# Kernel tuning notes

Hardware: AMD Instinct MI355X
Metric: run time of the kernel (lower is better)

Reference implementation:

```python
import jax, jax.numpy as jnp
import numpy as np

D = 1024
N_HEADS = 16
D_HEAD = D // N_HEADS


def setup_inputs() -> dict:
    key = jax.random.key(0)
    ks = jax.random.split(key, 7)
    B, S = 4, 1024
    x = jax.random.normal(ks[0], (B, S, D), dtype=jnp.float32)
    # per-head linear params, stacked over heads: W[h] is [d_head, d_head] (torch Linear weight),
    # y = s @ W[h].T + b[h]
    scale = 1.0 / np.sqrt(D_HEAD)
    Wq = jax.random.uniform(ks[1], (N_HEADS, D_HEAD, D_HEAD), jnp.float32, -scale, scale)
    Wk = jax.random.uniform(ks[2], (N_HEADS, D_HEAD, D_HEAD), jnp.float32, -scale, scale)
    Wv = jax.random.uniform(ks[3], (N_HEADS, D_HEAD, D_HEAD), jnp.float32, -scale, scale)
    bq = jax.random.uniform(ks[4], (N_HEADS, D_HEAD), jnp.float32, -scale, scale)
    bk = jax.random.uniform(ks[5], (N_HEADS, D_HEAD), jnp.float32, -scale, scale)
    bv = jax.random.uniform(ks[6], (N_HEADS, D_HEAD), jnp.float32, -scale, scale)
    return {"pix_sequences": x, "Wq": Wq, "Wk": Wk, "Wv": Wv,
            "bq": bq, "bk": bk, "bv": bv}


def reference(pix_sequences, Wq, Wk, Wv, bq, bk, bv):
    B, S, d = pix_sequences.shape
    # split feature dim into heads: [B, S, H, dh]
    xh = pix_sequences.reshape(B, S, N_HEADS, D_HEAD)
    # per-head linear: y = s @ W.T + b
    q = jnp.einsum('bshd,hed->bshe', xh, Wq) + bq  # [B,S,H,dh]
    k = jnp.einsum('bshd,hed->bshe', xh, Wk) + bk
    v = jnp.einsum('bshd,hed->bshe', xh, Wv) + bv
    scores = jnp.einsum('bqhd,bkhd->bhqk', q, k) / jnp.sqrt(jnp.float32(D_HEAD))
    attn = jax.nn.softmax(scores, axis=-1)  # [B,H,S,S]
    out = jnp.einsum('bhqk,bkhd->bqhd', attn, v)  # [B,S,H,dh]
    return out.reshape(B, S, d)
```

## Files before the change

### kernel.cpp

```cpp
#include <hip/hip_runtime.h>
#include <hip/hip_bf16.h>

constexpr int BB = 4;
constexpr int SS = 1024;
constexpr int HH = 16;
constexpr int DH = 64;
constexpr int DM = 1024;

using f32x16 = __attribute__((ext_vector_type(16))) float;
using s16x8  = __attribute__((ext_vector_type(8))) short;

__device__ __forceinline__ f32x16 mfma32(s16x8 a, s16x8 b, f32x16 c) {
    return __builtin_amdgcn_mfma_f32_32x32x16_bf16(a, b, c, 0, 0, 0);
}

__device__ __forceinline__ unsigned short bf16bits(float x) {
    union { __hip_bfloat16 h; unsigned short s; } cv;
    cv.h = __float2bfloat16(x);
    return cv.s;
}
__device__ __forceinline__ unsigned pk_bf16(float lo, float hi) {
    return (unsigned)bf16bits(lo) | ((unsigned)bf16bits(hi) << 16);
}

__device__ __forceinline__ float fast_exp2(float x) {
#if __has_builtin(__builtin_amdgcn_exp2f)
    return __builtin_amdgcn_exp2f(x);
#else
    return __expf(x * 0.6931471805599453f);
#endif
}

__device__ __forceinline__ int kperm(int g) {
    const int m = g & 12;
    return (m == 4 || m == 8) ? (g ^ 12) : g;
}

__global__ __launch_bounds__(256) void qkv_proj_kernel(
    const float* __restrict__ x,
    const float* __restrict__ Wq, const float* __restrict__ Wk, const float* __restrict__ Wv,
    const float* __restrict__ bq, const float* __restrict__ bk, const float* __restrict__ bv,
    __hip_bfloat16* __restrict__ q_ws, __hip_bfloat16* __restrict__ k_ws,
    __hip_bfloat16* __restrict__ v_ws)
{
    const int bid  = blockIdx.x;
    const int tile = bid & 7;
    const int pair = bid >> 3;
    const int b = pair >> 4, h = pair & 15;
    const int t = threadIdx.x;
    const int w = t >> 6, l = t & 63;
    const int lq = l & 31, hi = l >> 5;
    const int s0 = tile * 128;

    __shared__ __align__(16) char Xs[16384];
    __shared__ __align__(16) char Kt[16384];
    __shared__ __align__(16) char Vt[16384];

    {
        const float* xb = x + (size_t)(b * SS + s0) * DM + h * DH;
        #pragma unroll
        for (int i = 0; i < 8; ++i) {
            const int c  = t + 256 * i;
            const int r  = c >> 4, cw = c & 15;
            float4 v4 = *reinterpret_cast<const float4*>(xb + (size_t)r * DM + cw * 4);
            uint2 p;
            p.x = pk_bf16(v4.x, v4.y);
            p.y = pk_bf16(v4.z, v4.w);
            *reinterpret_cast<uint2*>(Xs + r * 128 + ((cw * 8) ^ ((r & 7) << 4))) = p;
        }
    }
    __syncthreads();

    const int arow = w * 32 + lq;
    const int asw  = (arow & 7) << 4;
    s16x8 af[4];
    #pragma unroll
    for (int s = 0; s < 4; ++s)
        af[s] = *reinterpret_cast<const s16x8*>(Xs + arow * 128 + ((s * 32 + hi * 16) ^ asw));
    __syncthreads();

    #pragma unroll
    for (int m = 0; m < 3; ++m) {
        const float* Wm = (m == 0) ? Wq : (m == 1) ? Wk : Wv;
        const float* bm = (m == 0) ? bq : (m == 1) ? bk : bv;

        f32x16 a0, a1;
        #pragma unroll
        for (int r = 0; r < 16; ++r) { a0[r] = 0.0f; a1[r] = 0.0f; }

        #pragma unroll
        for (int s = 0; s < 4; ++s) {
            const float* wp0 = Wm + (size_t)(h * DH + lq) * DH + s * 16 + hi * 8;
            const float* wp1 = wp0 + 32 * DH;
            float4 wa0 = reinterpret_cast<const float4*>(wp0)[0];
            float4 wb0 = reinterpret_cast<const float4*>(wp0)[1];
            float4 wa1 = reinterpret_cast<const float4*>(wp1)[0];
            float4 wb1 = reinterpret_cast<const float4*>(wp1)[1];
            union { unsigned u[4]; s16x8 v; } bf0, bf1;
            bf0.u[0] = pk_bf16(wa0.x, wa0.y); bf0.u[1] = pk_bf16(wa0.z, wa0.w);
            bf0.u[2] = pk_bf16(wb0.x, wb0.y); bf0.u[3] = pk_bf16(wb0.z, wb0.w);
            bf1.u[0] = pk_bf16(wa1.x, wa1.y); bf1.u[1] = pk_bf16(wa1.z, wa1.w);
            bf1.u[2] = pk_bf16(wb1.x, wb1.y); bf1.u[3] = pk_bf16(wb1.z, wb1.w);
            a0 = mfma32(af[s], bf0.v, a0);
            a1 = mfma32(af[s], bf1.v, a1);
        }

        const float bias0 = bm[h * DH + lq];
        const float bias1 = bm[h * DH + 32 + lq];

        if (m < 2) {
            char* T = (m == 0) ? Xs : Kt;
            #pragma unroll
            for (int r = 0; r < 16; ++r) {
                const int row = w * 32 + (r & 3) + 8 * (r >> 2) + 4 * hi;
                const int sw  = (row & 7) << 4;
                *reinterpret_cast<unsigned short*>(T + row * 128 + ((lq * 2) ^ sw)) =
                    bf16bits(a0[r] + bias0);
                *reinterpret_cast<unsigned short*>(T + row * 128 + (((32 + lq) * 2) ^ sw)) =
                    bf16bits(a1[r] + bias1);
            }
        } else {
            #pragma unroll
            for (int g = 0; g < 4; ++g) {
                const int off = w * 64 + g * 16 + hi * 8;
                uint2 p0, p1;
                p0.x = pk_bf16(a0[4*g+0] + bias0, a0[4*g+1] + bias0);
                p0.y = pk_bf16(a0[4*g+2] + bias0, a0[4*g+3] + bias0);
                p1.x = pk_bf16(a1[4*g+0] + bias1, a1[4*g+1] + bias1);
                p1.y = pk_bf16(a1[4*g+2] + bias1, a1[4*g+3] + bias1);
                *reinterpret_cast<uint2*>(Vt + lq * 256 + (off ^ ((lq & 7) << 4))) = p0;
                *reinterpret_cast<uint2*>(Vt + (32 + lq) * 256 + (off ^ (((32 + lq) & 7) << 4))) = p1;
            }
        }
    }
    __syncthreads();

    #pragma unroll
    for (int i = 0; i < 4; ++i) {
        const int c   = t + 256 * i;
        const int row = c >> 3, cc = c & 7;
        const int off = row * 128 + ((cc * 16) ^ ((row & 7) << 4));
        s16x8 qv = *reinterpret_cast<const s16x8*>(Xs + off);
        *reinterpret_cast<s16x8*>(q_ws + ((size_t)pair * SS + s0 + row) * DH + cc * 8) = qv;
        s16x8 kv = *reinterpret_cast<const s16x8*>(Kt + off);
        *reinterpret_cast<s16x8*>(k_ws + ((size_t)pair * SS + s0 + row) * DH + cc * 8) = kv;
    }
    #pragma unroll
    for (int i = 0; i < 4; ++i) {
        const int c   = t + 256 * i;
        const int row = c >> 4, cc = c & 15;
        s16x8 vv = *reinterpret_cast<const s16x8*>(
            Vt + row * 256 + ((cc * 16) ^ ((row & 7) << 4)));
        *reinterpret_cast<s16x8*>(v_ws + ((size_t)pair * DH + row) * SS + s0 + cc * 8) = vv;
    }
}

__global__ __launch_bounds__(512, 4) void attn_kernel(
    const __hip_bfloat16* __restrict__ q_ws,
    const __hip_bfloat16* __restrict__ k_ws,
    const __hip_bfloat16* __restrict__ v_ws,
    float* __restrict__ out)
{
    const int bid  = blockIdx.x;
    const int lbid = (bid & 7) * 64 + (bid >> 3);
    const int qt   = lbid & 7;
    const int pair = lbid >> 3;
    const int b = pair >> 4, h = pair & 15;
    const int t = threadIdx.x;
    const int w = t >> 6, l = t & 63;
    const int lq = l & 31, hi = l >> 5;
    const int qg = w & 3, p = w >> 2;

    __shared__ __align__(16) char smem[33792];

    const __hip_bfloat16* qp =
        q_ws + ((size_t)pair * SS + qt * 128 + qg * 32 + lq) * DH + hi * 8;
    s16x8 qf[4];
    #pragma unroll
    for (int s5 = 0; s5 < 4; ++s5)
        qf[s5] = *reinterpret_cast<const s16x8*>(qp + s5 * 16);

    const int u0 = t, u1 = t + 512;
    const __hip_bfloat16* kb = k_ws + (size_t)pair * SS * DH;
    const __hip_bfloat16* vb = v_ws + (size_t)pair * DH * SS;

    const int r0g = (u0 >> 3) & 31, r0m = r0g & 12;
    const int pr0 = (u0 >> 3 & ~31) | ((r0m == 4 || r0m == 8) ? (r0g ^ 12) : r0g);
    const int kOff0 = pr0 * 128 + (((u0 & 7) ^ (pr0 & 7)) << 4);
    const int r1g = (u1 >> 3) & 31, r1m = r1g & 12;
    const int pr1 = (u1 >> 3 & ~31) | ((r1m == 4 || r1m == 8) ? (r1g ^ 12) : r1g);
    const int kOff1 = pr1 * 128 + (((u1 & 7) ^ (pr1 & 7)) << 4);

    const int vOff0 = (u0 >> 4) * 256 + (((u0 & 15) ^ ((u0 >> 4) & 15)) << 4);
    const int vOff1 = (u1 >> 4) * 256 + (((u1 & 15) ^ ((u1 >> 4) & 15)) << 4);
    const size_t vs0 = (size_t)(u0 >> 4) * SS + (u0 & 15) * 8;
    const size_t vs1 = (size_t)(u1 >> 4) * SS + (u1 & 15) * 8;

    {
        s16x8 k0 = *reinterpret_cast<const s16x8*>(kb + u0 * 8);
        s16x8 k1 = *reinterpret_cast<const s16x8*>(kb + u1 * 8);
        s16x8 v0 = *reinterpret_cast<const s16x8*>(vb + vs0);
        s16x8 v1 = *reinterpret_cast<const s16x8*>(vb + vs1);
        *reinterpret_cast<s16x8*>(smem + kOff0) = k0;
        *reinterpret_cast<s16x8*>(smem + kOff1) = k1;
        *reinterpret_cast<s16x8*>(smem + 16384 + vOff0) = v0;
        *reinterpret_cast<s16x8*>(smem + 16384 + vOff1) = v1;
    }
    __syncthreads();

    f32x16 o0, o1, lacc;
    #pragma unroll
    for (int r = 0; r < 16; ++r) { o0[r] = 0.0f; o1[r] = 0.0f; lacc[r] = 0.0f; }
    const float cml = 0.18033688011112042f;

    const int kbase0 = (p * 64 + lq) * 128;
    const int kbase1 = kbase0 + 32 * 128;
    const int swzK = (lq & 7) << 4;
    const int swzV = (lq & 15) << 4;
    const int vrow0 = lq * 256, vrow1 = (32 + lq) * 256;

    s16x8 kr0, kr1, vr0, vr1;
    for (int st = 0; st < 8; ++st) {
        if (st < 7) {
            kr0 = *reinterpret_cast<const s16x8*>(kb + (st + 1) * 8192 + u0 * 8);
            kr1 = *reinterpret_cast<const s16x8*>(kb + (st + 1) * 8192 + u1 * 8);
            vr0 = *reinterpret_cast<const s16x8*>(vb + vs0 + (st + 1) * 128);
            vr1 = *reinterpret_cast<const s16x8*>(vb + vs1 + (st + 1) * 128);
        }
        const char* Kp = smem;
        const char* Vp = smem + 16384;

        f32x16 sc0, sc1;
        #pragma unroll
        for (int r = 0; r < 16; ++r) { sc0[r] = 0.0f; sc1[r] = 0.0f; }
        #pragma unroll
        for (int s5 = 0; s5 < 4; ++s5) {
            const int co = (2 * s5 + hi) << 4;
            s16x8 ka = *reinterpret_cast<const s16x8*>(Kp + kbase0 + (co ^ swzK));
            sc0 = mfma32(ka, qf[s5], sc0);
        }
        #pragma unroll
        for (int s5 = 0; s5 < 4; ++s5) {
            const int co = (2 * s5 + hi) << 4;
            s16x8 ka = *reinterpret_cast<const s16x8*>(Kp + kbase1 + (co ^ swzK));
            sc1 = mfma32(ka, qf[s5], sc1);
        }

        #pragma unroll
        for (int r = 0; r < 16; ++r) {
            sc0[r] = fast_exp2(sc0[r] * cml);
            sc1[r] = fast_exp2(sc1[r] * cml);
            lacc[r] += sc0[r] + sc1[r];
        }

        #pragma unroll
        for (int s5 = 0; s5 < 4; ++s5) {
            const int base = (s5 & 1) * 8;
            union { unsigned u[4]; s16x8 v; } afr;
            if (s5 < 2) {
                afr.u[0] = pk_bf16(sc0[base + 0], sc0[base + 1]);
                afr.u[1] = pk_bf16(sc0[base + 2], sc0[base + 3]);
                afr.u[2] = pk_bf16(sc0[base + 4], sc0[base + 5]);
                afr.u[3] = pk_bf16(sc0[base + 6], sc0[base + 7]);
            } else {
                afr.u[0] = pk_bf16(sc1[base + 0], sc1[base + 1]);
                afr.u[1] = pk_bf16(sc1[base + 2], sc1[base + 3]);
                afr.u[2] = pk_bf16(sc1[base + 4], sc1[base + 5]);
                afr.u[3] = pk_bf16(sc1[base + 6], sc1[base + 7]);
            }
            const int co = (2 * s5 + hi) << 4;
            s16x8 vb0 = *reinterpret_cast<const s16x8*>(Vp + vrow0 + ((p * 128 + co) ^ swzV));
            o0 = mfma32(afr.v, vb0, o0);
            s16x8 vb1 = *reinterpret_cast<const s16x8*>(Vp + vrow1 + ((p * 128 + co) ^ swzV));
            o1 = mfma32(afr.v, vb1, o1);
        }

        __syncthreads();
        if (st < 7) {
            *reinterpret_cast<s16x8*>(smem + kOff0) = kr0;
            *reinterpret_cast<s16x8*>(smem + kOff1) = kr1;
            *reinterpret_cast<s16x8*>(smem + 16384 + vOff0) = vr0;
            *reinterpret_cast<s16x8*>(smem + 16384 + vOff1) = vr1;
            __syncthreads();
        }
    }

    float ts[16];
    #pragma unroll
    for (int r = 0; r < 16; ++r) ts[r] = lacc[r];
    #pragma unroll
    for (int s = 8; s >= 1; s >>= 1)
        #pragma unroll
        for (int r = 0; r < 8; ++r)
            if (r < s) ts[r] += ts[r + s];
    const float lsum = ts[0] + __shfl_xor(ts[0], 32);

    float* Obuf = reinterpret_cast<float*>(smem + qg * 8192);
    float* mlb  = reinterpret_cast<float*>(smem + 32768 + qg * 256);
    if (p == 1) {
        #pragma unroll
        for (int r = 0; r < 16; ++r) {
            const int qr = (r & 3) + 8 * (r >> 2) + 4 * hi;
            Obuf[qr * 64 + lq]      = o0[r];
            Obuf[qr * 64 + 32 + lq] = o1[r];
        }
        mlb[lq] = lsum;
    }
    __syncthreads();
    if (p == 0) {
        const float inv = 1.0f / (lsum + mlb[lq]);
        #pragma unroll
        for (int r = 0; r < 16; ++r) {
            const int qr = (r & 3) + 8 * (r >> 2) + 4 * hi;
            const float invr = __shfl(inv, qr);
            float* op = out + ((size_t)b * SS + qt * 128 + qg * 32 + qr) * DM + h * DH + lq;
            op[0]  = (o0[r] + Obuf[qr * 64 + lq])      * invr;
            op[32] = (o1[r] + Obuf[qr * 64 + 32 + lq]) * invr;
        }
    }
}

extern "C" void kernel_launch(void* const* d_in, const int* in_sizes, int n_in,
                              void* d_out, int out_size, void* d_ws, size_t ws_size,
                              hipStream_t stream) {
    const float* x  = (const float*)d_in[0];
    const float* Wq = (const float*)d_in[1];
    const float* Wk = (const float*)d_in[2];
    const float* Wv = (const float*)d_in[3];
    const float* bq = (const float*)d_in[4];
    const float* bk = (const float*)d_in[5];
    const float* bv = (const float*)d_in[6];
    float* out = (float*)d_out;

    __hip_bfloat16* q_ws = (__hip_bfloat16*)d_ws;
    __hip_bfloat16* k_ws = q_ws + (size_t)BB * HH * SS * DH;
    __hip_bfloat16* v_ws = k_ws + (size_t)BB * HH * SS * DH;

    qkv_proj_kernel<<<dim3(BB * HH * (SS / 128)), dim3(256), 0, stream>>>(
        x, Wq, Wk, Wv, bq, bk, bv, q_ws, k_ws, v_ws);
    attn_kernel<<<dim3(BB * HH * (SS / 64 / 2)), dim3(512), 0, stream>>>(
        q_ws, k_ws, v_ws, out);
}
```

Measured before the change: 50.97 us.

## Halve projection tile to 64 rows, split output columns across waves, add MFMA priority hints

The QKV projection kernel now processes 64 sequence rows per block instead of 128, with the four waves arranged as 2 row groups by 2 output-column halves, each computing one 32x32 MFMA accumulator. This doubles the grid to 1024 blocks and shrinks shared memory and registers per block, aiming at better occupancy and load balance on the projection stage. Weight fragments are reloaded by more blocks in exchange. The attention kernel also wraps its two MFMA phases in s_setprio raises so waves in matrix work get issue priority over waves doing exp and stores.

```diff
diff --git a/kernel.cpp b/kernel.cpp
--- a/kernel.cpp
+++ b/kernel.cpp
@@ -44,22 +44,23 @@
     __hip_bfloat16* __restrict__ v_ws)
 {
     const int bid  = blockIdx.x;
-    const int tile = bid & 7;
-    const int pair = bid >> 3;
+    const int tile = bid & 15;
+    const int pair = bid >> 4;
     const int b = pair >> 4, h = pair & 15;
     const int t = threadIdx.x;
     const int w = t >> 6, l = t & 63;
     const int lq = l & 31, hi = l >> 5;
-    const int s0 = tile * 128;
-
-    __shared__ __align__(16) char Xs[16384];
-    __shared__ __align__(16) char Kt[16384];
-    __shared__ __align__(16) char Vt[16384];
+    const int rg = w & 1, eh = w >> 1;
+    const int s0 = tile * 64;
+
+    __shared__ __align__(16) char Xs[8192];
+    __shared__ __align__(16) char Kt[8192];
+    __shared__ __align__(16) char Vt[8192];
 
     {
         const float* xb = x + (size_t)(b * SS + s0) * DM + h * DH;
         #pragma unroll
-        for (int i = 0; i < 8; ++i) {
+        for (int i = 0; i < 4; ++i) {
             const int c  = t + 256 * i;
             const int r  = c >> 4, cw = c & 15;
             float4 v4 = *reinterpret_cast<const float4*>(xb + (size_t)r * DM + cw * 4);
@@ -71,72 +72,61 @@
     }
     __syncthreads();
 
-    const int arow = w * 32 + lq;
+    const int arow = rg * 32 + lq;
     const int asw  = (arow & 7) << 4;
     s16x8 af[4];
     #pragma unroll
     for (int s = 0; s < 4; ++s)
         af[s] = *reinterpret_cast<const s16x8*>(Xs + arow * 128 + ((s * 32 + hi * 16) ^ asw));
     __syncthreads();
+
+    const int e = eh * 32 + lq;
 
     #pragma unroll
     for (int m = 0; m < 3; ++m) {
         const float* Wm = (m == 0) ? Wq : (m == 1) ? Wk : Wv;
         const float* bm = (m == 0) ? bq : (m == 1) ? bk : bv;
 
-        f32x16 a0, a1;
-        #pragma unroll
-        for (int r = 0; r < 16; ++r) { a0[r] = 0.0f; a1[r] = 0.0f; }
+        f32x16 acc;
+        #pragma unroll
+        for (int r = 0; r < 16; ++r) acc[r] = 0.0f;
 
         #pragma unroll
         for (int s = 0; s < 4; ++s) {
-            const float* wp0 = Wm + (size_t)(h * DH + lq) * DH + s * 16 + hi * 8;
-            const float* wp1 = wp0 + 32 * DH;
-            float4 wa0 = reinterpret_cast<const float4*>(wp0)[0];
-            float4 wb0 = reinterpret_cast<const float4*>(wp0)[1];
-            float4 wa1 = reinterpret_cast<const float4*>(wp1)[0];
-            float4 wb1 = reinterpret_cast<const float4*>(wp1)[1];
-            union { unsigned u[4]; s16x8 v; } bf0, bf1;
-            bf0.u[0] = pk_bf16(wa0.x, wa0.y); bf0.u[1] = pk_bf16(wa0.z, wa0.w);
-            bf0.u[2] = pk_bf16(wb0.x, wb0.y); bf0.u[3] = pk_bf16(wb0.z, wb0.w);
-            bf1.u[0] = pk_bf16(wa1.x, wa1.y); bf1.u[1] = pk_bf16(wa1.z, wa1.w);
-            bf1.u[2] = pk_bf16(wb1.x, wb1.y); bf1.u[3] = pk_bf16(wb1.z, wb1.w);
-            a0 = mfma32(af[s], bf0.v, a0);
-            a1 = mfma32(af[s], bf1.v, a1);
-        }
-
-        const float bias0 = bm[h * DH + lq];
-        const float bias1 = bm[h * DH + 32 + lq];
+            const float* wp = Wm + (size_t)(h * DH + e) * DH + s * 16 + hi * 8;
+            float4 wa = reinterpret_cast<const float4*>(wp)[0];
+            float4 wb = reinterpret_cast<const float4*>(wp)[1];
+            union { unsigned u[4]; s16x8 v; } bf;
+            bf.u[0] = pk_bf16(wa.x, wa.y); bf.u[1] = pk_bf16(wa.z, wa.w);
+            bf.u[2] = pk_bf16(wb.x, wb.y); bf.u[3] = pk_bf16(wb.z, wb.w);
+            acc = mfma32(af[s], bf.v, acc);
+        }
+
+        const float bias = bm[h * DH + e];
 
         if (m < 2) {
             char* T = (m == 0) ? Xs : Kt;
             #pragma unroll
             for (int r = 0; r < 16; ++r) {
-                const int row = w * 32 + (r & 3) + 8 * (r >> 2) + 4 * hi;
-                const int sw  = (row & 7) << 4;
-                *reinterpret_cast<unsigned short*>(T + row * 128 + ((lq * 2) ^ sw)) =
-                    bf16bits(a0[r] + bias0);
-                *reinterpret_cast<unsigned short*>(T + row * 128 + (((32 + lq) * 2) ^ sw)) =
-                    bf16bits(a1[r] + bias1);
+                const int row = rg * 32 + (r & 3) + 8 * (r >> 2) + 4 * hi;
+                *reinterpret_cast<unsigned short*>(
+                    T + row * 128 + ((e * 2) ^ ((row & 7) << 4))) = bf16bits(acc[r] + bias);
             }
         } else {
             #pragma unroll
             for (int g = 0; g < 4; ++g) {
-                const int off = w * 64 + g * 16 + hi * 8;
-                uint2 p0, p1;
-                p0.x = pk_bf16(a0[4*g+0] + bias0, a0[4*g+1] + bias0);
-                p0.y = pk_bf16(a0[4*g+2] + bias0, a0[4*g+3] + bias0);
-                p1.x = pk_bf16(a1[4*g+0] + bias1, a1[4*g+1] + bias1);
-                p1.y = pk_bf16(a1[4*g+2] + bias1, a1[4*g+3] + bias1);
-                *reinterpret_cast<uint2*>(Vt + lq * 256 + (off ^ ((lq & 7) << 4))) = p0;
-                *reinterpret_cast<uint2*>(Vt + (32 + lq) * 256 + (off ^ (((32 + lq) & 7) << 4))) = p1;
+                const int off = rg * 64 + g * 16 + hi * 8;
+                uint2 p0;
+                p0.x = pk_bf16(acc[4*g+0] + bias, acc[4*g+1] + bias);
+                p0.y = pk_bf16(acc[4*g+2] + bias, acc[4*g+3] + bias);
+                *reinterpret_cast<uint2*>(Vt + e * 128 + (off ^ ((e & 7) << 4))) = p0;
             }
         }
     }
     __syncthreads();
 
     #pragma unroll
-    for (int i = 0; i < 4; ++i) {
+    for (int i = 0; i < 2; ++i) {
         const int c   = t + 256 * i;
         const int row = c >> 3, cc = c & 7;
         const int off = row * 128 + ((cc * 16) ^ ((row & 7) << 4));
@@ -144,13 +134,7 @@
         *reinterpret_cast<s16x8*>(q_ws + ((size_t)pair * SS + s0 + row) * DH + cc * 8) = qv;
         s16x8 kv = *reinterpret_cast<const s16x8*>(Kt + off);
         *reinterpret_cast<s16x8*>(k_ws + ((size_t)pair * SS + s0 + row) * DH + cc * 8) = kv;
-    }
-    #pragma unroll
-    for (int i = 0; i < 4; ++i) {
-        const int c   = t + 256 * i;
-        const int row = c >> 4, cc = c & 15;
-        s16x8 vv = *reinterpret_cast<const s16x8*>(
-            Vt + row * 256 + ((cc * 16) ^ ((row & 7) << 4)));
+        s16x8 vv = *reinterpret_cast<const s16x8*>(Vt + off);
         *reinterpret_cast<s16x8*>(v_ws + ((size_t)pair * DH + row) * SS + s0 + cc * 8) = vv;
     }
 }
@@ -233,6 +217,7 @@
         f32x16 sc0, sc1;
         #pragma unroll
         for (int r = 0; r < 16; ++r) { sc0[r] = 0.0f; sc1[r] = 0.0f; }
+        __builtin_amdgcn_s_setprio(1);
         #pragma unroll
         for (int s5 = 0; s5 < 4; ++s5) {
             const int co = (2 * s5 + hi) << 4;
@@ -245,6 +230,7 @@
             s16x8 ka = *reinterpret_cast<const s16x8*>(Kp + kbase1 + (co ^ swzK));
             sc1 = mfma32(ka, qf[s5], sc1);
         }
+        __builtin_amdgcn_s_setprio(0);
 
         #pragma unroll
         for (int r = 0; r < 16; ++r) {
@@ -253,6 +239,7 @@
             lacc[r] += sc0[r] + sc1[r];
         }
 
+        __builtin_amdgcn_s_setprio(1);
         #pragma unroll
         for (int s5 = 0; s5 < 4; ++s5) {
             const int base = (s5 & 1) * 8;
@@ -274,6 +261,7 @@
             s16x8 vb1 = *reinterpret_cast<const s16x8*>(Vp + vrow1 + ((p * 128 + co) ^ swzV));
             o1 = mfma32(afr.v, vb1, o1);
         }
+        __builtin_amdgcn_s_setprio(0);
 
         __syncthreads();
         if (st < 7) {
@@ -336,7 +324,7 @@
     __hip_bfloat16* k_ws = q_ws + (size_t)BB * HH * SS * DH;
     __hip_bfloat16* v_ws = k_ws + (size_t)BB * HH * SS * DH;
 
-    qkv_proj_kernel<<<dim3(BB * HH * (SS / 128)), dim3(256), 0, stream>>>(
+    qkv_proj_kernel<<<dim3(BB * HH * (SS / 64)), dim3(256), 0, stream>>>(
         x, Wq, Wk, Wv, bq, bk, bv, q_ws, k_ws, v_ws);
     attn_kernel<<<dim3(BB * HH * (SS / 64 / 2)), dim3(512), 0, stream>>>(
         q_ws, k_ws, v_ws, out);
```

After: 54.28 us. 1.07x slower.

## Double-buffer K/V tiles in shared memory to remove per-step barrier

Applied to the files above, without the earlier changes.

Grows LDS to two 32KB K/V buffers and alternates between them each step. The next tile's prefetched registers are written to the other buffer mid-iteration, after the softmax exponentials, which removes the second __syncthreads per step and the serialized store phase. In exchange LDS per block roughly doubles to about 65KB. With 512-thread blocks and launch_bounds(512,4), this may cut how many blocks fit on a CU and so lower occupancy.

```diff
diff --git a/kernel.cpp b/kernel.cpp
--- a/kernel.cpp
+++ b/kernel.cpp
@@ -171,7 +171,7 @@
     const int lq = l & 31, hi = l >> 5;
     const int qg = w & 3, p = w >> 2;
 
-    __shared__ __align__(16) char smem[33792];
+    __shared__ __align__(16) char smem[66560];
 
     const __hip_bfloat16* qp =
         q_ws + ((size_t)pair * SS + qt * 128 + qg * 32 + lq) * DH + hi * 8;
@@ -191,8 +191,8 @@
     const int pr1 = (u1 >> 3 & ~31) | ((r1m == 4 || r1m == 8) ? (r1g ^ 12) : r1g);
     const int kOff1 = pr1 * 128 + (((u1 & 7) ^ (pr1 & 7)) << 4);
 
-    const int vOff0 = (u0 >> 4) * 256 + (((u0 & 15) ^ ((u0 >> 4) & 15)) << 4);
-    const int vOff1 = (u1 >> 4) * 256 + (((u1 & 15) ^ ((u1 >> 4) & 15)) << 4);
+    const int vOff0 = 16384 + (u0 >> 4) * 256 + (((u0 & 15) ^ ((u0 >> 4) & 15)) << 4);
+    const int vOff1 = 16384 + (u1 >> 4) * 256 + (((u1 & 15) ^ ((u1 >> 4) & 15)) << 4);
     const size_t vs0 = (size_t)(u0 >> 4) * SS + (u0 & 15) * 8;
     const size_t vs1 = (size_t)(u1 >> 4) * SS + (u1 & 15) * 8;
 
@@ -203,8 +203,8 @@
         s16x8 v1 = *reinterpret_cast<const s16x8*>(vb + vs1);
         *reinterpret_cast<s16x8*>(smem + kOff0) = k0;
         *reinterpret_cast<s16x8*>(smem + kOff1) = k1;
-        *reinterpret_cast<s16x8*>(smem + 16384 + vOff0) = v0;
-        *reinterpret_cast<s16x8*>(smem + 16384 + vOff1) = v1;
+        *reinterpret_cast<s16x8*>(smem + vOff0) = v0;
+        *reinterpret_cast<s16x8*>(smem + vOff1) = v1;
     }
     __syncthreads();
 
@@ -217,18 +217,19 @@
     const int kbase1 = kbase0 + 32 * 128;
     const int swzK = (lq & 7) << 4;
     const int swzV = (lq & 15) << 4;
-    const int vrow0 = lq * 256, vrow1 = (32 + lq) * 256;
-
-    s16x8 kr0, kr1, vr0, vr1;
+    const int vrow0 = 16384 + lq * 256, vrow1 = 16384 + (32 + lq) * 256;
+
     for (int st = 0; st < 8; ++st) {
+        const char* cur = smem + (st & 1) * 32768;
+        char* nxt = smem + ((st + 1) & 1) * 32768;
+
+        s16x8 kr0, kr1, vr0, vr1;
         if (st < 7) {
             kr0 = *reinterpret_cast<const s16x8*>(kb + (st + 1) * 8192 + u0 * 8);
             kr1 = *reinterpret_cast<const s16x8*>(kb + (st + 1) * 8192 + u1 * 8);
             vr0 = *reinterpret_cast<const s16x8*>(vb + vs0 + (st + 1) * 128);
             vr1 = *reinterpret_cast<const s16x8*>(vb + vs1 + (st + 1) * 128);
         }
-        const char* Kp = smem;
-        const char* Vp = smem + 16384;
 
         f32x16 sc0, sc1;
         #pragma unroll
@@ -236,13 +237,13 @@
         #pragma unroll
         for (int s5 = 0; s5 < 4; ++s5) {
             const int co = (2 * s5 + hi) << 4;
-            s16x8 ka = *reinterpret_cast<const s16x8*>(Kp + kbase0 + (co ^ swzK));
+            s16x8 ka = *reinterpret_cast<const s16x8*>(cur + kbase0 + (co ^ swzK));
             sc0 = mfma32(ka, qf[s5], sc0);
         }
         #pragma unroll
         for (int s5 = 0; s5 < 4; ++s5) {
             const int co = (2 * s5 + hi) << 4;
-            s16x8 ka = *reinterpret_cast<const s16x8*>(Kp + kbase1 + (co ^ swzK));
+            s16x8 ka = *reinterpret_cast<const s16x8*>(cur + kbase1 + (co ^ swzK));
             sc1 = mfma32(ka, qf[s5], sc1);
         }
 
@@ -251,6 +252,13 @@
             sc0[r] = fast_exp2(sc0[r] * cml);
             sc1[r] = fast_exp2(sc1[r] * cml);
             lacc[r] += sc0[r] + sc1[r];
+        }
+
+        if (st < 7) {
+            *reinterpret_cast<s16x8*>(nxt + kOff0) = kr0;
+            *reinterpret_cast<s16x8*>(nxt + kOff1) = kr1;
+            *reinterpret_cast<s16x8*>(nxt + vOff0) = vr0;
+            *reinterpret_cast<s16x8*>(nxt + vOff1) = vr1;
         }
 
         #pragma unroll
@@ -269,20 +277,13 @@
                 afr.u[3] = pk_bf16(sc1[base + 6], sc1[base + 7]);
             }
             const int co = (2 * s5 + hi) << 4;
-            s16x8 vb0 = *reinterpret_cast<const s16x8*>(Vp + vrow0 + ((p * 128 + co) ^ swzV));
+            s16x8 vb0 = *reinterpret_cast<const s16x8*>(cur + vrow0 + ((p * 128 + co) ^ swzV));
             o0 = mfma32(afr.v, vb0, o0);
-            s16x8 vb1 = *reinterpret_cast<const s16x8*>(Vp + vrow1 + ((p * 128 + co) ^ swzV));
+            s16x8 vb1 = *reinterpret_cast<const s16x8*>(cur + vrow1 + ((p * 128 + co) ^ swzV));
             o1 = mfma32(afr.v, vb1, o1);
         }
 
         __syncthreads();
-        if (st < 7) {
-            *reinterpret_cast<s16x8*>(smem + kOff0) = kr0;
-            *reinterpret_cast<s16x8*>(smem + kOff1) = kr1;
-            *reinterpret_cast<s16x8*>(smem + 16384 + vOff0) = vr0;
-            *reinterpret_cast<s16x8*>(smem + 16384 + vOff1) = vr1;
-            __syncthreads();
-        }
     }
 
     float ts[16];
@@ -296,7 +297,7 @@
     const float lsum = ts[0] + __shfl_xor(ts[0], 32);
 
     float* Obuf = reinterpret_cast<float*>(smem + qg * 8192);
-    float* mlb  = reinterpret_cast<float*>(smem + 32768 + qg * 256);
+    float* mlb  = reinterpret_cast<float*>(smem + 65536 + qg * 256);
     if (p == 1) {
         #pragma unroll
         for (int r = 0; r < 16; ++r) {
```

Result: slower. 55.88 us (+9.6%).
